# Kernel tuning notes

Measured on AMD Instinct MI355X. Metric: run time of the kernel, lower is better.

## Reference

```python
import jax, jax.numpy as jnp
import numpy as np

E, K, NG, TG = 64, 8, 8, 4   # num_experts, top_k, num_expert_group, topk_group
CAP = 1024
SCALE = 2.5                   # routed_scaling_factor


def setup_inputs() -> dict:
    key = jax.random.key(0)
    ks = jax.random.split(key, 9)
    B, S, H, F = 1, 2048, 1024, 512
    bound = 1.0 / 32.0  # kaiming_uniform(a=sqrt(5)) on [E, H]: sqrt(6/(6*H))
    return {
        "hidden_states": jax.random.normal(ks[0], (B, S, H), jnp.float32),
        "gate_weight": jax.random.uniform(ks[1], (E, H), jnp.float32, -bound, bound),
        "e_bias": jnp.zeros((E,), jnp.float32),
        "w1": jax.random.normal(ks[2], (E, F, H), jnp.float32) * 0.02,
        "w2": jax.random.normal(ks[3], (E, H, F), jnp.float32) * 0.02,
        "w3": jax.random.normal(ks[4], (E, F, H), jnp.float32) * 0.02,
        "shared_gate": jax.random.normal(ks[5], (2 * F, H), jnp.float32) * 0.02,
        "shared_up": jax.random.normal(ks[6], (2 * F, H), jnp.float32) * 0.02,
        "shared_down": jax.random.normal(ks[7], (H, 2 * F), jnp.float32) * 0.02,
    }


def _route(x_flat, gate_weight, e_bias):
    T = x_flat.shape[0]
    logits = x_flat.astype(jnp.float32) @ gate_weight.astype(jnp.float32).T  # [T,E]
    scores = jax.nn.sigmoid(logits)
    sfc = scores + e_bias[None, :]
    # group-limited routing: keep TG of NG groups by sum of top-2 scores per group
    group_scores = jax.lax.top_k(sfc.reshape(T, NG, E // NG), 2)[0].sum(-1)  # [T,NG]
    _, gidx = jax.lax.top_k(group_scores, TG)
    gmask = jnp.zeros((T, NG), jnp.float32).at[jnp.arange(T)[:, None], gidx].set(1.0)
    smask = jnp.repeat(gmask, E // NG, axis=1)  # [T,E]
    tmp = jnp.where(smask > 0, sfc, 0.0)
    _, topk_idx = jax.lax.top_k(tmp, K)  # [T,K]
    topk_w = jnp.take_along_axis(scores, topk_idx, axis=1)
    topk_w = topk_w / (topk_w.sum(-1, keepdims=True) + 1e-20)
    return topk_idx, topk_w * SCALE


def _moe_forward(hidden_states, gate_weight, e_bias, w1, w2, w3,
                 shared_gate, shared_up, shared_down):
    B, S, H = hidden_states.shape
    T = B * S
    x = hidden_states.reshape(T, H)
    topk_idx, topk_w = _route(x, gate_weight, e_bias)

    # --- dispatch: sort slots by expert, compute position within expert ---
    Sk = T * K
    flat_e = topk_idx.reshape(-1)                      # [Sk]
    order = jnp.argsort(flat_e)                        # stable sort
    sorted_e = flat_e[order]
    counts = jax.ops.segment_sum(jnp.ones((Sk,), jnp.int32), flat_e, num_segments=E)
    offsets = jnp.cumsum(counts) - counts              # exclusive prefix
    pos = jnp.arange(Sk) - offsets[sorted_e]           # position within expert
    tok_sorted = x[order // K]                         # [Sk,H]

    xe = jnp.zeros((E, CAP, H), x.dtype).at[sorted_e, pos].set(tok_sorted, mode="drop")
    # --- grouped SwiGLU expert MLP ---
    h = jax.nn.silu(jnp.einsum("ech,efh->ecf", xe, w1)) * jnp.einsum("ech,efh->ecf", xe, w3)
    ye = jnp.einsum("ecf,ehf->ech", h, w2)             # [E,CAP,H]

    # --- combine: gather back, weight, scatter-add per token ---
    pos_c = jnp.minimum(pos, CAP - 1)
    vals = ye[sorted_e, pos_c]
    vals = jnp.where((pos < CAP)[:, None], vals, 0.0)
    flat_w = topk_w.reshape(-1)[order].astype(vals.dtype)
    flat_t = (jnp.arange(Sk) // K)[order]
    out = jax.ops.segment_sum(vals * flat_w[:, None], flat_t, num_segments=T)

    # --- shared expert (SwiGLU MLP over all tokens) ---
    shared = (jax.nn.silu(x @ shared_gate.T) * (x @ shared_up.T)) @ shared_down.T
    return (out + shared).reshape(B, S, H)


def reference(hidden_states, gate_weight, e_bias, w1, w2, w3,
              shared_gate, shared_up, shared_down):
    return _moe_forward(hidden_states, gate_weight, e_bias, w1, w2, w3,
                        shared_gate, shared_up, shared_down)
```

## Files before the change

### kernel.cpp

```cpp
#include <hip/hip_runtime.h>

#define T_TOK 2048
#define HDIM  1024
#define FDIM  512
#define NEXP  64
#define TOPK  8
#define NGRP  8
#define TGRP  4
#define CAPC  1024
#define SCALE_F 2.5f

typedef _Float16 f16;
typedef _Float16 f16x4 __attribute__((ext_vector_type(4)));
typedef _Float16 f16x8 __attribute__((ext_vector_type(8)));
typedef float    f32x4 __attribute__((ext_vector_type(4)));

typedef const __attribute__((address_space(1))) void* gas_t;
typedef __attribute__((address_space(3))) void* las_t;
__device__ __forceinline__ void gl2lds16(const void* g, void* l) {
    __builtin_amdgcn_global_load_lds((gas_t)g, (las_t)l, 16, 0, 0);
}
#define FRAG(S, r, s) (*(const f16x8*)&S[(r)*64 + (((s) ^ ((r)&7)))*8])

__global__ void k_cvt(const float* __restrict__ src, f16* __restrict__ dst, int n8)
{
    int i = blockIdx.x * blockDim.x + threadIdx.x;
    if (i >= n8) return;
    const float4* s = (const float4*)src + (size_t)i * 2;
    float4 a = s[0], b = s[1];
    f16x8 h = { (f16)a.x, (f16)a.y, (f16)a.z, (f16)a.w,
                (f16)b.x, (f16)b.y, (f16)b.z, (f16)b.w };
    *(f16x8*)(dst + (size_t)i * 8) = h;
}

__global__ __launch_bounds__(256) void k_logits(const float* __restrict__ x,
                                                const float* __restrict__ gw,
                                                float* __restrict__ logits)
{
    __shared__ float sX[8][132];
    __shared__ float sGW[64][132];
    int tid = threadIdx.x;
    int t0 = blockIdx.x * 8;
    int tl = tid & 7;
    int eb = tid >> 3;
    f32x4 acc0 = {0.f,0.f,0.f,0.f}, acc1 = {0.f,0.f,0.f,0.f};

    for (int hc0 = 0; hc0 < HDIM; hc0 += 128) {
        __syncthreads();
        {
            int row = tid >> 5, c4 = tid & 31;
            float4 v = *(const float4*)(x + (size_t)(t0 + row) * HDIM + hc0 + c4 * 4);
            *(float4*)&sX[row][c4 * 4] = v;
        }
        #pragma unroll
        for (int k = 0; k < 8; ++k) {
            int row = k * 8 + (tid >> 5), c4 = tid & 31;
            float4 v = *(const float4*)(gw + (size_t)row * HDIM + hc0 + c4 * 4);
            *(float4*)&sGW[row][c4 * 4] = v;
        }
        __syncthreads();
        #pragma unroll
        for (int c4 = 0; c4 < 32; ++c4) {
            float4 ax = *(const float4*)&sX[tl][c4 * 4];
            float4 g0 = *(const float4*)&sGW[eb][c4 * 4];
            float4 g1 = *(const float4*)&sGW[eb + 32][c4 * 4];
            acc0.x += ax.x * g0.x; acc0.y += ax.y * g0.y;
            acc0.z += ax.z * g0.z; acc0.w += ax.w * g0.w;
            acc1.x += ax.x * g1.x; acc1.y += ax.y * g1.y;
            acc1.z += ax.z * g1.z; acc1.w += ax.w * g1.w;
        }
    }
    float l0 = (acc0.x + acc0.y) + (acc0.z + acc0.w);
    float l1 = (acc1.x + acc1.y) + (acc1.z + acc1.w);
    logits[(size_t)(t0 + tl) * NEXP + eb]      = l0;
    logits[(size_t)(t0 + tl) * NEXP + eb + 32] = l1;
}

__global__ void k_topk(const float* __restrict__ logits, const float* __restrict__ ebias,
                       int* __restrict__ counts,
                       int* __restrict__ slot_e, int* __restrict__ slot_pos,
                       float* __restrict__ slot_w)
{
    int t = blockIdx.x;
    int lane = threadIdx.x;
    __shared__ float sS[NEXP], sF[NEXP];
    __shared__ float gsc[NGRP];
    __shared__ unsigned gmask_s;
    __shared__ int sIdx[TOPK];

    float logit = logits[(size_t)t * NEXP + lane];
    float score = 1.f / (1.f + __expf(-logit));
    float sfc = score + ebias[lane];
    sS[lane] = score; sF[lane] = sfc;
    __syncthreads();

    if (lane < NGRP) {
        float m1 = -1e30f, m2 = -1e30f;
        for (int j = 0; j < NEXP / NGRP; ++j) {
            float v = sF[lane * (NEXP / NGRP) + j];
            if (v > m1) { m2 = m1; m1 = v; } else if (v > m2) m2 = v;
        }
        gsc[lane] = m1 + m2;
    }
    __syncthreads();
    if (lane == 0) {
        unsigned gm = 0;
        for (int s = 0; s < TGRP; ++s) {
            float best = -1e30f; int bg = 0;
            for (int g = 0; g < NGRP; ++g)
                if (!((gm >> g) & 1) && gsc[g] > best) { best = gsc[g]; bg = g; }
            gm |= 1u << bg;
        }
        gmask_s = gm;
    }
    __syncthreads();

    float vv = ((gmask_s >> (lane >> 3)) & 1) ? sfc : 0.0f;
    for (int k = 0; k < TOPK; ++k) {
        float bv = vv; int bi = lane;
        for (int off = 32; off; off >>= 1) {
            float ov = __shfl_down(bv, off);
            int   oi = __shfl_down(bi, off);
            if (ov > bv || (ov == bv && oi < bi)) { bv = ov; bi = oi; }
        }
        bi = __shfl(bi, 0);
        if (lane == bi) vv = -1e30f;
        if (lane == 0) sIdx[k] = bi;
    }
    __syncthreads();
    if (lane == 0) {
        float sum = 0.f;
        for (int k = 0; k < TOPK; ++k) sum += sS[sIdx[k]];
        float inv = SCALE_F / (sum + 1e-20f);
        for (int k = 0; k < TOPK; ++k) {
            int e = sIdx[k];
            int pos = atomicAdd(&counts[e], 1);
            int s = t * TOPK + k;
            slot_e[s] = e; slot_pos[s] = pos; slot_w[s] = sS[e] * inv;
        }
    }
}

__global__ void k_scan(const int* __restrict__ counts, int* __restrict__ offsets)
{
    if (threadIdx.x == 0) {
        int s = 0;
        for (int e = 0; e < NEXP; ++e) { offsets[e] = s; s += counts[e]; }
    }
}

__global__ void k_rowmap(const int* __restrict__ slot_e, const int* __restrict__ slot_pos,
                         const int* __restrict__ offsets, int* __restrict__ row_tok)
{
    int s = blockIdx.x * 256 + threadIdx.x;
    if (s >= T_TOK * TOPK) return;
    int p = slot_pos[s];
    if (p >= CAPC) return;
    row_tok[offsets[slot_e[s]] + p] = s >> 3;
}

__global__ __launch_bounds__(256, 2) void k_gateup(
    const f16* __restrict__ A, const f16* __restrict__ W1,
    const f16* __restrict__ W3, f16* __restrict__ Hout,
    const int* __restrict__ offsets, const int* __restrict__ counts,
    const int* __restrict__ row_tok,
    int K, int Nld, int Mtot, int expert_mode)
{
    int e = expert_mode ? blockIdx.z : 0;
    int rowbeg = expert_mode ? offsets[e] : 0;
    int M = expert_mode ? (counts[e] < CAPC ? counts[e] : CAPC) : Mtot;
    int mtile = blockIdx.y * 128;
    if (mtile >= M) return;
    int Mblk = M - mtile; if (Mblk > 128) Mblk = 128;
    int n0 = blockIdx.x * 64;
    const f16* W1e = W1 + (size_t)e * Nld * K;
    const f16* W3e = W3 + (size_t)e * Nld * K;

    __shared__ __align__(16) f16 sA[128 * 64];
    __shared__ __align__(16) f16 sB1[64 * 64];
    __shared__ __align__(16) f16 sB3[64 * 64];

    int tid = threadIdx.x, wave = tid >> 6, lane = tid & 63;
    int subrow = lane >> 3;
    int lseg = (lane & 7) ^ subrow;

    const f16* aptr[4];
    #pragma unroll
    for (int c = 0; c < 4; ++c) {
        int r = (wave * 4 + c) * 8 + subrow;
        int rr = (r < Mblk) ? r : 0;
        size_t srow = expert_mode ? (size_t)row_tok[rowbeg + mtile + rr]
                                  : (size_t)(rowbeg + mtile + rr);
        aptr[c] = A + srow * (size_t)K + lseg * 8;
    }
    const f16 *b1ptr[2], *b3ptr[2];
    #pragma unroll
    for (int c = 0; c < 2; ++c) {
        int r = (wave * 2 + c) * 8 + subrow;
        b1ptr[c] = W1e + (size_t)(n0 + r) * K + lseg * 8;
        b3ptr[c] = W3e + (size_t)(n0 + r) * K + lseg * 8;
    }

    int lrow = lane & 15, lquad = lane >> 4;
    int wm = (wave & 1) * 64, wn = (wave >> 1) * 32;

    f32x4 accg[4][2], accu[4][2];
    #pragma unroll
    for (int i = 0; i < 4; ++i)
        #pragma unroll
        for (int j = 0; j < 2; ++j) {
            f32x4 z = {0.f, 0.f, 0.f, 0.f};
            accg[i][j] = z; accu[i][j] = z;
        }

    for (int k0 = 0; k0 < K; k0 += 64) {
        #pragma unroll
        for (int c = 0; c < 4; ++c)
            gl2lds16(aptr[c] + k0, &sA[(wave * 4 + c) * 512]);
        #pragma unroll
        for (int c = 0; c < 2; ++c) {
            gl2lds16(b1ptr[c] + k0, &sB1[(wave * 2 + c) * 512]);
            gl2lds16(b3ptr[c] + k0, &sB3[(wave * 2 + c) * 512]);
        }
        __syncthreads();
        #pragma unroll
        for (int ks = 0; ks < 2; ++ks) {
            int seg = ks * 4 + lquad;
            f16x8 a[4], b1[2], b3[2];
            #pragma unroll
            for (int i = 0; i < 4; ++i) a[i] = FRAG(sA, wm + i * 16 + lrow, seg);
            #pragma unroll
            for (int j = 0; j < 2; ++j) {
                b1[j] = FRAG(sB1, wn + j * 16 + lrow, seg);
                b3[j] = FRAG(sB3, wn + j * 16 + lrow, seg);
            }
            #pragma unroll
            for (int i = 0; i < 4; ++i)
                #pragma unroll
                for (int j = 0; j < 2; ++j) {
                    accg[i][j] = __builtin_amdgcn_mfma_f32_16x16x32_f16(a[i], b1[j], accg[i][j], 0, 0, 0);
                    accu[i][j] = __builtin_amdgcn_mfma_f32_16x16x32_f16(a[i], b3[j], accu[i][j], 0, 0, 0);
                }
        }
        __syncthreads();
    }

    f16* Hrow = Hout + (size_t)(rowbeg + mtile) * Nld + n0;
    #pragma unroll
    for (int i = 0; i < 4; ++i)
        #pragma unroll
        for (int j = 0; j < 2; ++j)
            #pragma unroll
            for (int r = 0; r < 4; ++r) {
                int m = wm + i * 16 + lquad * 4 + r;
                if (m < Mblk) {
                    int n = wn + j * 16 + lrow;
                    float g = accg[i][j][r], u = accu[i][j][r];
                    float h = g / (1.f + __expf(-g)) * u;
                    Hrow[(size_t)m * Nld + n] = (f16)h;
                }
            }
}

__global__ __launch_bounds__(256, 2) void k_down(
    const f16* __restrict__ A, const f16* __restrict__ W,
    f16* __restrict__ Y,
    const int* __restrict__ offsets, const int* __restrict__ counts,
    int K, int Nld, int Mtot, int expert_mode)
{
    int e = expert_mode ? blockIdx.z : 0;
    int rowbeg = expert_mode ? offsets[e] : 0;
    int M = expert_mode ? (counts[e] < CAPC ? counts[e] : CAPC) : Mtot;
    int mtile = blockIdx.y * 128;
    if (mtile >= M) return;
    int Mblk = M - mtile; if (Mblk > 128) Mblk = 128;
    int n0 = blockIdx.x * 128;
    const f16* We = W + (size_t)e * Nld * K;

    __shared__ __align__(16) f16 sA[128 * 64];
    __shared__ __align__(16) f16 sW[128 * 64];

    int tid = threadIdx.x, wave = tid >> 6, lane = tid & 63;
    int subrow = lane >> 3;
    int lseg = (lane & 7) ^ subrow;

    const f16 *aptr[4], *wptr[4];
    #pragma unroll
    for (int c = 0; c < 4; ++c) {
        int r = (wave * 4 + c) * 8 + subrow;
        int rr = (r < Mblk) ? r : 0;
        aptr[c] = A + (size_t)(rowbeg + mtile + rr) * K + lseg * 8;
        wptr[c] = We + (size_t)(n0 + r) * K + lseg * 8;
    }

    int lrow = lane & 15, lquad = lane >> 4;
    int wm = (wave & 1) * 64, wn = (wave >> 1) * 64;

    f32x4 acc[4][4];
    #pragma unroll
    for (int i = 0; i < 4; ++i)
        #pragma unroll
        for (int j = 0; j < 4; ++j) { f32x4 z = {0.f, 0.f, 0.f, 0.f}; acc[i][j] = z; }

    for (int k0 = 0; k0 < K; k0 += 64) {
        #pragma unroll
        for (int c = 0; c < 4; ++c) {
            gl2lds16(aptr[c] + k0, &sA[(wave * 4 + c) * 512]);
            gl2lds16(wptr[c] + k0, &sW[(wave * 4 + c) * 512]);
        }
        __syncthreads();
        #pragma unroll
        for (int ks = 0; ks < 2; ++ks) {
            int seg = ks * 4 + lquad;
            f16x8 a[4], b[4];
            #pragma unroll
            for (int i = 0; i < 4; ++i) a[i] = FRAG(sA, wm + i * 16 + lrow, seg);
            #pragma unroll
            for (int j = 0; j < 4; ++j) b[j] = FRAG(sW, wn + j * 16 + lrow, seg);
            #pragma unroll
            for (int i = 0; i < 4; ++i)
                #pragma unroll
                for (int j = 0; j < 4; ++j)
                    acc[i][j] = __builtin_amdgcn_mfma_f32_16x16x32_f16(a[i], b[j], acc[i][j], 0, 0, 0);
        }
        __syncthreads();
    }

    f16* Yrow = Y + (size_t)(rowbeg + mtile) * Nld + n0;
    #pragma unroll
    for (int i = 0; i < 4; ++i)
        #pragma unroll
        for (int j = 0; j < 4; ++j)
            #pragma unroll
            for (int r = 0; r < 4; ++r) {
                int m = wm + i * 16 + lquad * 4 + r;
                if (m < Mblk)
                    Yrow[(size_t)m * Nld + wn + j * 16 + lrow] = (f16)acc[i][j][r];
            }
}

__global__ void k_combine(const f16* __restrict__ y, const f16* __restrict__ ys,
                          const int* __restrict__ slot_e, const int* __restrict__ slot_pos,
                          const float* __restrict__ slot_w, const int* __restrict__ offsets,
                          float* __restrict__ out)
{
    int t = blockIdx.x, i = threadIdx.x;
    size_t col = (size_t)i * 4;
    f16x4 s = *(const f16x4*)(ys + (size_t)t * HDIM + col);
    float a0 = (float)s[0], a1 = (float)s[1], a2 = (float)s[2], a3 = (float)s[3];
    #pragma unroll
    for (int k = 0; k < TOPK; ++k) {
        int sidx = t * TOPK + k;
        int p = slot_pos[sidx];
        if (p < CAPC) {
            int row = offsets[slot_e[sidx]] + p;
            float w = slot_w[sidx];
            f16x4 v = *(const f16x4*)(y + (size_t)row * HDIM + col);
            a0 += w * (float)v[0]; a1 += w * (float)v[1];
            a2 += w * (float)v[2]; a3 += w * (float)v[3];
        }
    }
    float4 o = {a0, a1, a2, a3};
    *(float4*)(out + (size_t)t * HDIM + col) = o;
}

extern "C" void kernel_launch(void* const* d_in, const int* in_sizes, int n_in,
                              void* d_out, int out_size, void* d_ws, size_t ws_size,
                              hipStream_t stream)
{
    const float* x  = (const float*)d_in[0];
    const float* gw = (const float*)d_in[1];
    const float* eb = (const float*)d_in[2];
    const float* w1 = (const float*)d_in[3];
    const float* w2 = (const float*)d_in[4];
    const float* w3 = (const float*)d_in[5];
    const float* sg = (const float*)d_in[6];
    const float* su = (const float*)d_in[7];
    const float* sd = (const float*)d_in[8];
    float* out = (float*)d_out;

    char* p = (char*)d_ws;
    size_t off = 0;
    auto alloc = [&](size_t n) { void* r = p + off; off = (off + n + 255) & ~(size_t)255; return r; };
    int*   counts   = (int*)alloc(NEXP * 4);
    int*   offsets  = (int*)alloc(NEXP * 4);
    int*   slot_e   = (int*)alloc((size_t)T_TOK * TOPK * 4);
    int*   slot_pos = (int*)alloc((size_t)T_TOK * TOPK * 4);
    float* slot_w   = (float*)alloc((size_t)T_TOK * TOPK * 4);
    int*   row_tok  = (int*)alloc((size_t)T_TOK * TOPK * 4);
    float* logits   = (float*)alloc((size_t)T_TOK * NEXP * 4);
    f16*   xb  = (f16*)alloc((size_t)T_TOK * HDIM * 2);
    f16*   h   = (f16*)alloc((size_t)T_TOK * TOPK * FDIM * 2);
    f16*   y   = (f16*)alloc((size_t)T_TOK * TOPK * HDIM * 2);
    f16*   hs  = (f16*)alloc((size_t)T_TOK * 2 * FDIM * 2);
    f16*   ys  = (f16*)alloc((size_t)T_TOK * HDIM * 2);
    f16*   wbufA = (f16*)alloc((size_t)NEXP * FDIM * HDIM * 2);
    f16*   wbufB = (f16*)alloc((size_t)NEXP * FDIM * HDIM * 2);
    f16*   sgh = (f16*)alloc((size_t)2 * FDIM * HDIM * 2);
    f16*   suh = (f16*)alloc((size_t)2 * FDIM * HDIM * 2);
    f16*   sdh = (f16*)alloc((size_t)HDIM * 2 * FDIM * 2);

    hipMemsetAsync(counts, 0, NEXP * 4, stream);

    const int XW8 = T_TOK * HDIM / 8;
    k_cvt<<<(XW8 + 255) / 256, 256, 0, stream>>>(x, xb, XW8);
    k_logits<<<T_TOK / 8, 256, 0, stream>>>(x, gw, logits);
    k_topk<<<T_TOK, 64, 0, stream>>>(logits, eb, counts, slot_e, slot_pos, slot_w);
    k_scan<<<1, 64, 0, stream>>>(counts, offsets);
    k_rowmap<<<(T_TOK * TOPK + 255) / 256, 256, 0, stream>>>(slot_e, slot_pos, offsets, row_tok);

    const int EW8 = NEXP * FDIM * HDIM / 8;
    const int SW8 = 2 * FDIM * HDIM / 8;
    k_cvt<<<(EW8 + 255) / 256, 256, 0, stream>>>(w1, wbufA, EW8);
    k_cvt<<<(EW8 + 255) / 256, 256, 0, stream>>>(w3, wbufB, EW8);
    k_cvt<<<(SW8 + 255) / 256, 256, 0, stream>>>(sg, sgh, SW8);
    k_cvt<<<(SW8 + 255) / 256, 256, 0, stream>>>(su, suh, SW8);
    k_cvt<<<(SW8 + 255) / 256, 256, 0, stream>>>(sd, sdh, SW8);

    k_gateup<<<dim3(FDIM / 64, CAPC / 128, NEXP), 256, 0, stream>>>(
        xb, wbufA, wbufB, h, offsets, counts, row_tok, HDIM, FDIM, 0, 1);
    k_gateup<<<dim3((2 * FDIM) / 64, T_TOK / 128, 1), 256, 0, stream>>>(
        xb, sgh, suh, hs, offsets, counts, row_tok, HDIM, 2 * FDIM, T_TOK, 0);

    k_cvt<<<(EW8 + 255) / 256, 256, 0, stream>>>(w2, wbufA, EW8);

    k_down<<<dim3(HDIM / 128, CAPC / 128, NEXP), 256, 0, stream>>>(
        h, wbufA, y, offsets, counts, FDIM, HDIM, 0, 1);
    k_down<<<dim3(HDIM / 128, T_TOK / 128, 1), 256, 0, stream>>>(
        hs, sdh, ys, offsets, counts, 2 * FDIM, HDIM, T_TOK, 0);

    k_combine<<<T_TOK, 256, 0, stream>>>(y, ys, slot_e, slot_pos, slot_w, offsets, out);
}
```

Baseline: 695.6 us.

## Fuse fp32-to-f16 weight conversion into GEMM loads with double-buffered LDS

Removes the separate weight conversion kernels and has the gate/up and down GEMMs load fp32 weights directly, converting to f16 in registers before writing to LDS. The main loops become double-buffered so the next tile's loads overlap the current tile's MFMA work. This avoids writing and re-reading f16 weight copies, but each M-tile block now re-reads fp32 weights, which doubles per-block weight bytes and raises register and LDS use.

```diff
diff --git a/kernel.cpp b/kernel.cpp
--- a/kernel.cpp
+++ b/kernel.cpp
@@ -22,15 +22,19 @@
 }
 #define FRAG(S, r, s) (*(const f16x8*)&S[(r)*64 + (((s) ^ ((r)&7)))*8])
 
+__device__ __forceinline__ f16x8 cvt8(float4 a, float4 b) {
+    f16x8 h = { (f16)a.x, (f16)a.y, (f16)a.z, (f16)a.w,
+                (f16)b.x, (f16)b.y, (f16)b.z, (f16)b.w };
+    return h;
+}
+
 __global__ void k_cvt(const float* __restrict__ src, f16* __restrict__ dst, int n8)
 {
     int i = blockIdx.x * blockDim.x + threadIdx.x;
     if (i >= n8) return;
     const float4* s = (const float4*)src + (size_t)i * 2;
     float4 a = s[0], b = s[1];
-    f16x8 h = { (f16)a.x, (f16)a.y, (f16)a.z, (f16)a.w,
-                (f16)b.x, (f16)b.y, (f16)b.z, (f16)b.w };
-    *(f16x8*)(dst + (size_t)i * 8) = h;
+    *(f16x8*)(dst + (size_t)i * 8) = cvt8(a, b);
 }
 
 __global__ __launch_bounds__(256) void k_logits(const float* __restrict__ x,
@@ -160,8 +164,8 @@
 }
 
 __global__ __launch_bounds__(256, 2) void k_gateup(
-    const f16* __restrict__ A, const f16* __restrict__ W1,
-    const f16* __restrict__ W3, f16* __restrict__ Hout,
+    const f16* __restrict__ A, const float* __restrict__ W1,
+    const float* __restrict__ W3, f16* __restrict__ Hout,
     const int* __restrict__ offsets, const int* __restrict__ counts,
     const int* __restrict__ row_tok,
     int K, int Nld, int Mtot, int expert_mode)
@@ -173,12 +177,12 @@
     if (mtile >= M) return;
     int Mblk = M - mtile; if (Mblk > 128) Mblk = 128;
     int n0 = blockIdx.x * 64;
-    const f16* W1e = W1 + (size_t)e * Nld * K;
-    const f16* W3e = W3 + (size_t)e * Nld * K;
-
-    __shared__ __align__(16) f16 sA[128 * 64];
-    __shared__ __align__(16) f16 sB1[64 * 64];
-    __shared__ __align__(16) f16 sB3[64 * 64];
+    const float* W1e = W1 + (size_t)e * Nld * K;
+    const float* W3e = W3 + (size_t)e * Nld * K;
+
+    __shared__ __align__(16) f16 sA[2][128 * 64];
+    __shared__ __align__(16) f16 sB1[2][64 * 64];
+    __shared__ __align__(16) f16 sB3[2][64 * 64];
 
     int tid = threadIdx.x, wave = tid >> 6, lane = tid & 63;
     int subrow = lane >> 3;
@@ -193,12 +197,12 @@
                                   : (size_t)(rowbeg + mtile + rr);
         aptr[c] = A + srow * (size_t)K + lseg * 8;
     }
-    const f16 *b1ptr[2], *b3ptr[2];
+    const float *w1p[2], *w3p[2];
     #pragma unroll
     for (int c = 0; c < 2; ++c) {
         int r = (wave * 2 + c) * 8 + subrow;
-        b1ptr[c] = W1e + (size_t)(n0 + r) * K + lseg * 8;
-        b3ptr[c] = W3e + (size_t)(n0 + r) * K + lseg * 8;
+        w1p[c] = W1e + (size_t)(n0 + r) * K + lseg * 8;
+        w3p[c] = W3e + (size_t)(n0 + r) * K + lseg * 8;
     }
 
     int lrow = lane & 15, lquad = lane >> 4;
@@ -213,26 +217,43 @@
             accg[i][j] = z; accu[i][j] = z;
         }
 
-    for (int k0 = 0; k0 < K; k0 += 64) {
+    float4 r1[2][2], r3[2][2];
+
+    auto loadW = [&](int k0) {
+        #pragma unroll
+        for (int c = 0; c < 2; ++c) {
+            r1[c][0] = *(const float4*)(w1p[c] + k0);
+            r1[c][1] = *(const float4*)(w1p[c] + k0 + 4);
+            r3[c][0] = *(const float4*)(w3p[c] + k0);
+            r3[c][1] = *(const float4*)(w3p[c] + k0 + 4);
+        }
+    };
+    auto stageA = [&](int k0, int b) {
         #pragma unroll
         for (int c = 0; c < 4; ++c)
-            gl2lds16(aptr[c] + k0, &sA[(wave * 4 + c) * 512]);
+            gl2lds16(aptr[c] + k0, &sA[b][(wave * 4 + c) * 512]);
+    };
+    auto writeW = [&](int b) {
         #pragma unroll
         for (int c = 0; c < 2; ++c) {
-            gl2lds16(b1ptr[c] + k0, &sB1[(wave * 2 + c) * 512]);
-            gl2lds16(b3ptr[c] + k0, &sB3[(wave * 2 + c) * 512]);
-        }
-        __syncthreads();
+            *(f16x8*)&sB1[b][(wave * 2 + c) * 512 + lane * 8] = cvt8(r1[c][0], r1[c][1]);
+            *(f16x8*)&sB3[b][(wave * 2 + c) * 512 + lane * 8] = cvt8(r3[c][0], r3[c][1]);
+        }
+    };
+    auto compute = [&](int b) {
+        const f16* cA  = sA[b];
+        const f16* cB1 = sB1[b];
+        const f16* cB3 = sB3[b];
         #pragma unroll
         for (int ks = 0; ks < 2; ++ks) {
             int seg = ks * 4 + lquad;
             f16x8 a[4], b1[2], b3[2];
             #pragma unroll
-            for (int i = 0; i < 4; ++i) a[i] = FRAG(sA, wm + i * 16 + lrow, seg);
+            for (int i = 0; i < 4; ++i) a[i] = FRAG(cA, wm + i * 16 + lrow, seg);
             #pragma unroll
             for (int j = 0; j < 2; ++j) {
-                b1[j] = FRAG(sB1, wn + j * 16 + lrow, seg);
-                b3[j] = FRAG(sB3, wn + j * 16 + lrow, seg);
+                b1[j] = FRAG(cB1, wn + j * 16 + lrow, seg);
+                b3[j] = FRAG(cB3, wn + j * 16 + lrow, seg);
             }
             #pragma unroll
             for (int i = 0; i < 4; ++i)
@@ -242,8 +263,23 @@
                     accu[i][j] = __builtin_amdgcn_mfma_f32_16x16x32_f16(a[i], b3[j], accu[i][j], 0, 0, 0);
                 }
         }
+    };
+
+    loadW(0);
+    stageA(0, 0);
+    writeW(0);
+    __syncthreads();
+
+    int cb = 0;
+    for (int k0 = 64; k0 < K; k0 += 64) {
+        loadW(k0);
+        stageA(k0, cb ^ 1);
+        compute(cb);
+        writeW(cb ^ 1);
         __syncthreads();
-    }
+        cb ^= 1;
+    }
+    compute(cb);
 
     f16* Hrow = Hout + (size_t)(rowbeg + mtile) * Nld + n0;
     #pragma unroll
@@ -263,7 +299,7 @@
 }
 
 __global__ __launch_bounds__(256, 2) void k_down(
-    const f16* __restrict__ A, const f16* __restrict__ W,
+    const f16* __restrict__ A, const float* __restrict__ W,
     f16* __restrict__ Y,
     const int* __restrict__ offsets, const int* __restrict__ counts,
     int K, int Nld, int Mtot, int expert_mode)
@@ -275,22 +311,23 @@
     if (mtile >= M) return;
     int Mblk = M - mtile; if (Mblk > 128) Mblk = 128;
     int n0 = blockIdx.x * 128;
-    const f16* We = W + (size_t)e * Nld * K;
-
-    __shared__ __align__(16) f16 sA[128 * 64];
-    __shared__ __align__(16) f16 sW[128 * 64];
+    const float* We = W + (size_t)e * Nld * K;
+
+    __shared__ __align__(16) f16 sA[2][128 * 64];
+    __shared__ __align__(16) f16 sW[2][128 * 64];
 
     int tid = threadIdx.x, wave = tid >> 6, lane = tid & 63;
     int subrow = lane >> 3;
     int lseg = (lane & 7) ^ subrow;
 
-    const f16 *aptr[4], *wptr[4];
+    const f16* aptr[4];
+    const float* wp[4];
     #pragma unroll
     for (int c = 0; c < 4; ++c) {
         int r = (wave * 4 + c) * 8 + subrow;
         int rr = (r < Mblk) ? r : 0;
         aptr[c] = A + (size_t)(rowbeg + mtile + rr) * K + lseg * 8;
-        wptr[c] = We + (size_t)(n0 + r) * K + lseg * 8;
+        wp[c]   = We + (size_t)(n0 + r) * K + lseg * 8;
     }
 
     int lrow = lane & 15, lquad = lane >> 4;
@@ -302,29 +339,59 @@
         #pragma unroll
         for (int j = 0; j < 4; ++j) { f32x4 z = {0.f, 0.f, 0.f, 0.f}; acc[i][j] = z; }
 
-    for (int k0 = 0; k0 < K; k0 += 64) {
+    float4 wr[4][2];
+
+    auto loadW = [&](int k0) {
         #pragma unroll
         for (int c = 0; c < 4; ++c) {
-            gl2lds16(aptr[c] + k0, &sA[(wave * 4 + c) * 512]);
-            gl2lds16(wptr[c] + k0, &sW[(wave * 4 + c) * 512]);
-        }
-        __syncthreads();
+            wr[c][0] = *(const float4*)(wp[c] + k0);
+            wr[c][1] = *(const float4*)(wp[c] + k0 + 4);
+        }
+    };
+    auto stageA = [&](int k0, int b) {
+        #pragma unroll
+        for (int c = 0; c < 4; ++c)
+            gl2lds16(aptr[c] + k0, &sA[b][(wave * 4 + c) * 512]);
+    };
+    auto writeW = [&](int b) {
+        #pragma unroll
+        for (int c = 0; c < 4; ++c)
+            *(f16x8*)&sW[b][(wave * 4 + c) * 512 + lane * 8] = cvt8(wr[c][0], wr[c][1]);
+    };
+    auto compute = [&](int b) {
+        const f16* cA = sA[b];
+        const f16* cW = sW[b];
         #pragma unroll
         for (int ks = 0; ks < 2; ++ks) {
             int seg = ks * 4 + lquad;
-            f16x8 a[4], b[4];
-            #pragma unroll
-            for (int i = 0; i < 4; ++i) a[i] = FRAG(sA, wm + i * 16 + lrow, seg);
-            #pragma unroll
-            for (int j = 0; j < 4; ++j) b[j] = FRAG(sW, wn + j * 16 + lrow, seg);
+            f16x8 a[4], bb[4];
+            #pragma unroll
+            for (int i = 0; i < 4; ++i) a[i]  = FRAG(cA, wm + i * 16 + lrow, seg);
+            #pragma unroll
+            for (int j = 0; j < 4; ++j) bb[j] = FRAG(cW, wn + j * 16 + lrow, seg);
             #pragma unroll
             for (int i = 0; i < 4; ++i)
                 #pragma unroll
                 for (int j = 0; j < 4; ++j)
-                    acc[i][j] = __builtin_amdgcn_mfma_f32_16x16x32_f16(a[i], b[j], acc[i][j], 0, 0, 0);
-        }
+                    acc[i][j] = __builtin_amdgcn_mfma_f32_16x16x32_f16(a[i], bb[j], acc[i][j], 0, 0, 0);
+        }
+    };
+
+    loadW(0);
+    stageA(0, 0);
+    writeW(0);
+    __syncthreads();
+
+    int cb = 0;
+    for (int k0 = 64; k0 < K; k0 += 64) {
+        loadW(k0);
+        stageA(k0, cb ^ 1);
+        compute(cb);
+        writeW(cb ^ 1);
         __syncthreads();
-    }
+        cb ^= 1;
+    }
+    compute(cb);
 
     f16* Yrow = Y + (size_t)(rowbeg + mtile) * Nld + n0;
     #pragma unroll
@@ -394,11 +461,6 @@
     f16*   y   = (f16*)alloc((size_t)T_TOK * TOPK * HDIM * 2);
     f16*   hs  = (f16*)alloc((size_t)T_TOK * 2 * FDIM * 2);
     f16*   ys  = (f16*)alloc((size_t)T_TOK * HDIM * 2);
-    f16*   wbufA = (f16*)alloc((size_t)NEXP * FDIM * HDIM * 2);
-    f16*   wbufB = (f16*)alloc((size_t)NEXP * FDIM * HDIM * 2);
-    f16*   sgh = (f16*)alloc((size_t)2 * FDIM * HDIM * 2);
-    f16*   suh = (f16*)alloc((size_t)2 * FDIM * HDIM * 2);
-    f16*   sdh = (f16*)alloc((size_t)HDIM * 2 * FDIM * 2);
 
     hipMemsetAsync(counts, 0, NEXP * 4, stream);
 
@@ -409,25 +471,15 @@
     k_scan<<<1, 64, 0, stream>>>(counts, offsets);
     k_rowmap<<<(T_TOK * TOPK + 255) / 256, 256, 0, stream>>>(slot_e, slot_pos, offsets, row_tok);
 
-    const int EW8 = NEXP * FDIM * HDIM / 8;
-    const int SW8 = 2 * FDIM * HDIM / 8;
-    k_cvt<<<(EW8 + 255) / 256, 256, 0, stream>>>(w1, wbufA, EW8);
-    k_cvt<<<(EW8 + 255) / 256, 256, 0, stream>>>(w3, wbufB, EW8);
-    k_cvt<<<(SW8 + 255) / 256, 256, 0, stream>>>(sg, sgh, SW8);
-    k_cvt<<<(SW8 + 255) / 256, 256, 0, stream>>>(su, suh, SW8);
-    k_cvt<<<(SW8 + 255) / 256, 256, 0, stream>>>(sd, sdh, SW8);
-
     k_gateup<<<dim3(FDIM / 64, CAPC / 128, NEXP), 256, 0, stream>>>(
-        xb, wbufA, wbufB, h, offsets, counts, row_tok, HDIM, FDIM, 0, 1);
+        xb, w1, w3, h, offsets, counts, row_tok, HDIM, FDIM, 0, 1);
     k_gateup<<<dim3((2 * FDIM) / 64, T_TOK / 128, 1), 256, 0, stream>>>(
-        xb, sgh, suh, hs, offsets, counts, row_tok, HDIM, 2 * FDIM, T_TOK, 0);
-
-    k_cvt<<<(EW8 + 255) / 256, 256, 0, stream>>>(w2, wbufA, EW8);
+        xb, sg, su, hs, offsets, counts, row_tok, HDIM, 2 * FDIM, T_TOK, 0);
 
     k_down<<<dim3(HDIM / 128, CAPC / 128, NEXP), 256, 0, stream>>>(
-        h, wbufA, y, offsets, counts, FDIM, HDIM, 0, 1);
+        h, w2, y, offsets, counts, FDIM, HDIM, 0, 1);
     k_down<<<dim3(HDIM / 128, T_TOK / 128, 1), 256, 0, stream>>>(
-        hs, sdh, ys, offsets, counts, 2 * FDIM, HDIM, T_TOK, 0);
+        hs, sd, ys, offsets, counts, 2 * FDIM, HDIM, T_TOK, 0);
 
     k_combine<<<T_TOK, 256, 0, stream>>>(y, ys, slot_e, slot_pos, slot_w, offsets, out);
 }
```

Measured after the change: 687.6 us. No clear change (-1.1%).

## Fuse fp32-to-fp16 weight conversion into grouped GEMM loads with register prefetch

Applied to the files above, without the earlier changes.

Drops the separate conversion kernels for the expert and shared weights. The GEMM kernels now read the fp32 weights directly, convert them to fp16 in registers, and write them to LDS, with a software prefetch of the next K-chunk. Blocks grow to 512 threads with 256-row M tiles so each weight tile is reused across more tokens. This removes a full write and re-read of the fp16 weight copies, at the cost of reading fp32 weights inside the GEMM, higher register pressure from the prefetch, and lower occupancy per block.

```diff
diff --git a/kernel.cpp b/kernel.cpp
--- a/kernel.cpp
+++ b/kernel.cpp
@@ -22,15 +22,19 @@
 }
 #define FRAG(S, r, s) (*(const f16x8*)&S[(r)*64 + (((s) ^ ((r)&7)))*8])
 
+__device__ __forceinline__ f16x8 cvt8(float4 a, float4 b) {
+    f16x8 h = { (f16)a.x, (f16)a.y, (f16)a.z, (f16)a.w,
+                (f16)b.x, (f16)b.y, (f16)b.z, (f16)b.w };
+    return h;
+}
+
 __global__ void k_cvt(const float* __restrict__ src, f16* __restrict__ dst, int n8)
 {
     int i = blockIdx.x * blockDim.x + threadIdx.x;
     if (i >= n8) return;
     const float4* s = (const float4*)src + (size_t)i * 2;
     float4 a = s[0], b = s[1];
-    f16x8 h = { (f16)a.x, (f16)a.y, (f16)a.z, (f16)a.w,
-                (f16)b.x, (f16)b.y, (f16)b.z, (f16)b.w };
-    *(f16x8*)(dst + (size_t)i * 8) = h;
+    *(f16x8*)(dst + (size_t)i * 8) = cvt8(a, b);
 }
 
 __global__ __launch_bounds__(256) void k_logits(const float* __restrict__ x,
@@ -159,9 +163,9 @@
     row_tok[offsets[slot_e[s]] + p] = s >> 3;
 }
 
-__global__ __launch_bounds__(256, 2) void k_gateup(
-    const f16* __restrict__ A, const f16* __restrict__ W1,
-    const f16* __restrict__ W3, f16* __restrict__ Hout,
+__global__ __launch_bounds__(512, 4) void k_gateup(
+    const f16* __restrict__ A, const float* __restrict__ W1,
+    const float* __restrict__ W3, f16* __restrict__ Hout,
     const int* __restrict__ offsets, const int* __restrict__ counts,
     const int* __restrict__ row_tok,
     int K, int Nld, int Mtot, int expert_mode)
@@ -169,14 +173,14 @@
     int e = expert_mode ? blockIdx.z : 0;
     int rowbeg = expert_mode ? offsets[e] : 0;
     int M = expert_mode ? (counts[e] < CAPC ? counts[e] : CAPC) : Mtot;
-    int mtile = blockIdx.y * 128;
+    int mtile = blockIdx.y * 256;
     if (mtile >= M) return;
-    int Mblk = M - mtile; if (Mblk > 128) Mblk = 128;
+    int Mblk = M - mtile; if (Mblk > 256) Mblk = 256;
     int n0 = blockIdx.x * 64;
-    const f16* W1e = W1 + (size_t)e * Nld * K;
-    const f16* W3e = W3 + (size_t)e * Nld * K;
-
-    __shared__ __align__(16) f16 sA[128 * 64];
+    const float* W1e = W1 + (size_t)e * Nld * K;
+    const float* W3e = W3 + (size_t)e * Nld * K;
+
+    __shared__ __align__(16) f16 sA[256 * 64];
     __shared__ __align__(16) f16 sB1[64 * 64];
     __shared__ __align__(16) f16 sB3[64 * 64];
 
@@ -193,16 +197,11 @@
                                   : (size_t)(rowbeg + mtile + rr);
         aptr[c] = A + srow * (size_t)K + lseg * 8;
     }
-    const f16 *b1ptr[2], *b3ptr[2];
-    #pragma unroll
-    for (int c = 0; c < 2; ++c) {
-        int r = (wave * 2 + c) * 8 + subrow;
-        b1ptr[c] = W1e + (size_t)(n0 + r) * K + lseg * 8;
-        b3ptr[c] = W3e + (size_t)(n0 + r) * K + lseg * 8;
-    }
+    const float* w1p = W1e + (size_t)(n0 + wave * 8 + subrow) * K + lseg * 8;
+    const float* w3p = W3e + (size_t)(n0 + wave * 8 + subrow) * K + lseg * 8;
 
     int lrow = lane & 15, lquad = lane >> 4;
-    int wm = (wave & 1) * 64, wn = (wave >> 1) * 32;
+    int wm = (wave >> 1) * 64, wn = (wave & 1) * 32;
 
     f32x4 accg[4][2], accu[4][2];
     #pragma unroll
@@ -213,16 +212,15 @@
             accg[i][j] = z; accu[i][j] = z;
         }
 
-    for (int k0 = 0; k0 < K; k0 += 64) {
+    float4 a1_0, a1_1, a3_0, a3_1;
+    float4 b1_0, b1_1, b3_0, b3_1;
+
+    auto stageA = [&](int k0) {
         #pragma unroll
         for (int c = 0; c < 4; ++c)
             gl2lds16(aptr[c] + k0, &sA[(wave * 4 + c) * 512]);
-        #pragma unroll
-        for (int c = 0; c < 2; ++c) {
-            gl2lds16(b1ptr[c] + k0, &sB1[(wave * 2 + c) * 512]);
-            gl2lds16(b3ptr[c] + k0, &sB3[(wave * 2 + c) * 512]);
-        }
-        __syncthreads();
+    };
+    auto compute = [&]() {
         #pragma unroll
         for (int ks = 0; ks < 2; ++ks) {
             int seg = ks * 4 + lquad;
@@ -242,6 +240,29 @@
                     accu[i][j] = __builtin_amdgcn_mfma_f32_16x16x32_f16(a[i], b3[j], accu[i][j], 0, 0, 0);
                 }
         }
+    };
+
+    a1_0 = *(const float4*)(w1p);     a1_1 = *(const float4*)(w1p + 4);
+    a3_0 = *(const float4*)(w3p);     a3_1 = *(const float4*)(w3p + 4);
+
+    for (int k0 = 0; k0 < K; k0 += 128) {
+        b1_0 = *(const float4*)(w1p + k0 + 64); b1_1 = *(const float4*)(w1p + k0 + 68);
+        b3_0 = *(const float4*)(w3p + k0 + 64); b3_1 = *(const float4*)(w3p + k0 + 68);
+        *(f16x8*)&sB1[wave * 512 + lane * 8] = cvt8(a1_0, a1_1);
+        *(f16x8*)&sB3[wave * 512 + lane * 8] = cvt8(a3_0, a3_1);
+        stageA(k0);
+        __syncthreads();
+        compute();
+        __syncthreads();
+        if (k0 + 128 < K) {
+            a1_0 = *(const float4*)(w1p + k0 + 128); a1_1 = *(const float4*)(w1p + k0 + 132);
+            a3_0 = *(const float4*)(w3p + k0 + 128); a3_1 = *(const float4*)(w3p + k0 + 132);
+        }
+        *(f16x8*)&sB1[wave * 512 + lane * 8] = cvt8(b1_0, b1_1);
+        *(f16x8*)&sB3[wave * 512 + lane * 8] = cvt8(b3_0, b3_1);
+        stageA(k0 + 64);
+        __syncthreads();
+        compute();
         __syncthreads();
     }
 
@@ -262,8 +283,8 @@
             }
 }
 
-__global__ __launch_bounds__(256, 2) void k_down(
-    const f16* __restrict__ A, const f16* __restrict__ W,
+__global__ __launch_bounds__(512, 4) void k_down(
+    const f16* __restrict__ A, const float* __restrict__ W,
     f16* __restrict__ Y,
     const int* __restrict__ offsets, const int* __restrict__ counts,
     int K, int Nld, int Mtot, int expert_mode)
@@ -271,30 +292,31 @@
     int e = expert_mode ? blockIdx.z : 0;
     int rowbeg = expert_mode ? offsets[e] : 0;
     int M = expert_mode ? (counts[e] < CAPC ? counts[e] : CAPC) : Mtot;
-    int mtile = blockIdx.y * 128;
+    int mtile = blockIdx.y * 256;
     if (mtile >= M) return;
-    int Mblk = M - mtile; if (Mblk > 128) Mblk = 128;
+    int Mblk = M - mtile; if (Mblk > 256) Mblk = 256;
     int n0 = blockIdx.x * 128;
-    const f16* We = W + (size_t)e * Nld * K;
-
-    __shared__ __align__(16) f16 sA[128 * 64];
+    const float* We = W + (size_t)e * Nld * K;
+
+    __shared__ __align__(16) f16 sA[256 * 64];
     __shared__ __align__(16) f16 sW[128 * 64];
 
     int tid = threadIdx.x, wave = tid >> 6, lane = tid & 63;
     int subrow = lane >> 3;
     int lseg = (lane & 7) ^ subrow;
 
-    const f16 *aptr[4], *wptr[4];
+    const f16* aptr[4];
     #pragma unroll
     for (int c = 0; c < 4; ++c) {
         int r = (wave * 4 + c) * 8 + subrow;
         int rr = (r < Mblk) ? r : 0;
         aptr[c] = A + (size_t)(rowbeg + mtile + rr) * K + lseg * 8;
-        wptr[c] = We + (size_t)(n0 + r) * K + lseg * 8;
-    }
+    }
+    const float* wp0 = We + (size_t)(n0 + (wave * 2 + 0) * 8 + subrow) * K + lseg * 8;
+    const float* wp1 = We + (size_t)(n0 + (wave * 2 + 1) * 8 + subrow) * K + lseg * 8;
 
     int lrow = lane & 15, lquad = lane >> 4;
-    int wm = (wave & 1) * 64, wn = (wave >> 1) * 64;
+    int wm = (wave >> 1) * 64, wn = (wave & 1) * 64;
 
     f32x4 acc[4][4];
     #pragma unroll
@@ -302,27 +324,52 @@
         #pragma unroll
         for (int j = 0; j < 4; ++j) { f32x4 z = {0.f, 0.f, 0.f, 0.f}; acc[i][j] = z; }
 
-    for (int k0 = 0; k0 < K; k0 += 64) {
-        #pragma unroll
-        for (int c = 0; c < 4; ++c) {
+    float4 aw0_0, aw0_1, aw1_0, aw1_1;
+    float4 bw0_0, bw0_1, bw1_0, bw1_1;
+
+    auto stageA = [&](int k0) {
+        #pragma unroll
+        for (int c = 0; c < 4; ++c)
             gl2lds16(aptr[c] + k0, &sA[(wave * 4 + c) * 512]);
-            gl2lds16(wptr[c] + k0, &sW[(wave * 4 + c) * 512]);
-        }
-        __syncthreads();
+    };
+    auto compute = [&]() {
         #pragma unroll
         for (int ks = 0; ks < 2; ++ks) {
             int seg = ks * 4 + lquad;
-            f16x8 a[4], b[4];
-            #pragma unroll
-            for (int i = 0; i < 4; ++i) a[i] = FRAG(sA, wm + i * 16 + lrow, seg);
-            #pragma unroll
-            for (int j = 0; j < 4; ++j) b[j] = FRAG(sW, wn + j * 16 + lrow, seg);
+            f16x8 a[4], bb[4];
+            #pragma unroll
+            for (int i = 0; i < 4; ++i) a[i]  = FRAG(sA, wm + i * 16 + lrow, seg);
+            #pragma unroll
+            for (int j = 0; j < 4; ++j) bb[j] = FRAG(sW, wn + j * 16 + lrow, seg);
             #pragma unroll
             for (int i = 0; i < 4; ++i)
                 #pragma unroll
                 for (int j = 0; j < 4; ++j)
-                    acc[i][j] = __builtin_amdgcn_mfma_f32_16x16x32_f16(a[i], b[j], acc[i][j], 0, 0, 0);
-        }
+                    acc[i][j] = __builtin_amdgcn_mfma_f32_16x16x32_f16(a[i], bb[j], acc[i][j], 0, 0, 0);
+        }
+    };
+
+    aw0_0 = *(const float4*)(wp0);     aw0_1 = *(const float4*)(wp0 + 4);
+    aw1_0 = *(const float4*)(wp1);     aw1_1 = *(const float4*)(wp1 + 4);
+
+    for (int k0 = 0; k0 < K; k0 += 128) {
+        bw0_0 = *(const float4*)(wp0 + k0 + 64); bw0_1 = *(const float4*)(wp0 + k0 + 68);
+        bw1_0 = *(const float4*)(wp1 + k0 + 64); bw1_1 = *(const float4*)(wp1 + k0 + 68);
+        *(f16x8*)&sW[(wave * 2 + 0) * 512 + lane * 8] = cvt8(aw0_0, aw0_1);
+        *(f16x8*)&sW[(wave * 2 + 1) * 512 + lane * 8] = cvt8(aw1_0, aw1_1);
+        stageA(k0);
+        __syncthreads();
+        compute();
+        __syncthreads();
+        if (k0 + 128 < K) {
+            aw0_0 = *(const float4*)(wp0 + k0 + 128); aw0_1 = *(const float4*)(wp0 + k0 + 132);
+            aw1_0 = *(const float4*)(wp1 + k0 + 128); aw1_1 = *(const float4*)(wp1 + k0 + 132);
+        }
+        *(f16x8*)&sW[(wave * 2 + 0) * 512 + lane * 8] = cvt8(bw0_0, bw0_1);
+        *(f16x8*)&sW[(wave * 2 + 1) * 512 + lane * 8] = cvt8(bw1_0, bw1_1);
+        stageA(k0 + 64);
+        __syncthreads();
+        compute();
         __syncthreads();
     }
 
@@ -394,11 +441,6 @@
     f16*   y   = (f16*)alloc((size_t)T_TOK * TOPK * HDIM * 2);
     f16*   hs  = (f16*)alloc((size_t)T_TOK * 2 * FDIM * 2);
     f16*   ys  = (f16*)alloc((size_t)T_TOK * HDIM * 2);
-    f16*   wbufA = (f16*)alloc((size_t)NEXP * FDIM * HDIM * 2);
-    f16*   wbufB = (f16*)alloc((size_t)NEXP * FDIM * HDIM * 2);
-    f16*   sgh = (f16*)alloc((size_t)2 * FDIM * HDIM * 2);
-    f16*   suh = (f16*)alloc((size_t)2 * FDIM * HDIM * 2);
-    f16*   sdh = (f16*)alloc((size_t)HDIM * 2 * FDIM * 2);
 
     hipMemsetAsync(counts, 0, NEXP * 4, stream);
 
@@ -409,25 +451,15 @@
     k_scan<<<1, 64, 0, stream>>>(counts, offsets);
     k_rowmap<<<(T_TOK * TOPK + 255) / 256, 256, 0, stream>>>(slot_e, slot_pos, offsets, row_tok);
 
-    const int EW8 = NEXP * FDIM * HDIM / 8;
-    const int SW8 = 2 * FDIM * HDIM / 8;
-    k_cvt<<<(EW8 + 255) / 256, 256, 0, stream>>>(w1, wbufA, EW8);
-    k_cvt<<<(EW8 + 255) / 256, 256, 0, stream>>>(w3, wbufB, EW8);
-    k_cvt<<<(SW8 + 255) / 256, 256, 0, stream>>>(sg, sgh, SW8);
-    k_cvt<<<(SW8 + 255) / 256, 256, 0, stream>>>(su, suh, SW8);
-    k_cvt<<<(SW8 + 255) / 256, 256, 0, stream>>>(sd, sdh, SW8);
-
-    k_gateup<<<dim3(FDIM / 64, CAPC / 128, NEXP), 256, 0, stream>>>(
-        xb, wbufA, wbufB, h, offsets, counts, row_tok, HDIM, FDIM, 0, 1);
-    k_gateup<<<dim3((2 * FDIM) / 64, T_TOK / 128, 1), 256, 0, stream>>>(
-        xb, sgh, suh, hs, offsets, counts, row_tok, HDIM, 2 * FDIM, T_TOK, 0);
-
-    k_cvt<<<(EW8 + 255) / 256, 256, 0, stream>>>(w2, wbufA, EW8);
-
-    k_down<<<dim3(HDIM / 128, CAPC / 128, NEXP), 256, 0, stream>>>(
-        h, wbufA, y, offsets, counts, FDIM, HDIM, 0, 1);
-    k_down<<<dim3(HDIM / 128, T_TOK / 128, 1), 256, 0, stream>>>(
-        hs, sdh, ys, offsets, counts, 2 * FDIM, HDIM, T_TOK, 0);
+    k_gateup<<<dim3(FDIM / 64, CAPC / 256, NEXP), 512, 0, stream>>>(
+        xb, w1, w3, h, offsets, counts, row_tok, HDIM, FDIM, 0, 1);
+    k_gateup<<<dim3((2 * FDIM) / 64, T_TOK / 256, 1), 512, 0, stream>>>(
+        xb, sg, su, hs, offsets, counts, row_tok, HDIM, 2 * FDIM, T_TOK, 0);
+
+    k_down<<<dim3(HDIM / 128, CAPC / 256, NEXP), 512, 0, stream>>>(
+        h, w2, y, offsets, counts, FDIM, HDIM, 0, 1);
+    k_down<<<dim3(HDIM / 128, T_TOK / 256, 1), 512, 0, stream>>>(
+        hs, sd, ys, offsets, counts, 2 * FDIM, HDIM, T_TOK, 0);
 
     k_combine<<<T_TOK, 256, 0, stream>>>(y, ys, slot_e, slot_pos, slot_w, offsets, out);
 }
```

Measured after the change: 1.327 ms. +90.8%, slower.
